# Performance work log

Measured on AMD Instinct MI355X. Metric: run time of the kernel, lower is better.

## Reference

```python
import jax, jax.numpy as jnp
import numpy as np

B, L, D = 8, 2048, 1024
MASKED = -2.0 ** 31  # fp32 path of the torch code


def setup_inputs() -> dict:
    key = jax.random.key(0)
    ks = jax.random.split(key, 11)
    s = 1.0 / np.sqrt(D)
    return {
        "Q": jax.random.normal(ks[0], (B, L, D), jnp.float32),
        "K": jax.random.normal(ks[1], (B, L, D), jnp.float32),
        "V": jax.random.normal(ks[2], (B, L, D), jnp.float32),
        "Wq": jax.random.normal(ks[3], (D, D), jnp.float32) * s,
        "bq": jax.random.normal(ks[4], (D,), jnp.float32) * s,
        "Wk": jax.random.normal(ks[5], (D, D), jnp.float32) * s,
        "bk": jax.random.normal(ks[6], (D,), jnp.float32) * s,
        "Wv": jax.random.normal(ks[7], (D, D), jnp.float32) * s,
        "bv": jax.random.normal(ks[8], (D,), jnp.float32) * s,
        "q_mask": jax.random.randint(ks[9], (B, L), 0, 2, jnp.int32),
        "k_mask": jax.random.randint(ks[10], (B, L), 0, 2, jnp.int32),
    }


def reference(Q, K, V, Wq, bq, Wk, bk, Wv, bv, q_mask, k_mask):
    # with_projection=True: linear projections (torch Linear: x @ W.T + b)
    Qp = jnp.einsum("bld,ed->ble", Q, Wq) + bq
    Kp = jnp.einsum("bld,ed->ble", K, Wk) + bk
    Vp = jnp.einsum("bld,ed->ble", V, Wv) + bv
    # NOTE: source hard-sets scale = 1 after computing sqrt(d_hidden)
    e = jnp.einsum("bqd,bkd->bqk", Qp, Kp)            # [B, Lq, Lk]
    e = jnp.where(k_mask[:, None, :] == 0, MASKED, e)  # masked_fill on key axis
    a = jax.nn.softmax(e, axis=-1)                     # with_sparse=False
    # dropout is identity in eval/reference mode
    a = jnp.einsum("bqk,bkd->bqd", a, Vp)
    a = jnp.where(q_mask[:, :, None] == 0, 0.0, a)     # zero masked query rows
    return a, e
```

## Files before the change

### kernel.cpp

```cpp
#include <hip/hip_runtime.h>
#include <cstddef>
#include <cstdint>

constexpr int Bn = 8;
constexpr int Ln = 2048;
constexpr int Dn = 1024;
constexpr float MASKED_VAL = -2147483648.0f;

typedef unsigned short u16;
typedef unsigned int   u32;
typedef __attribute__((ext_vector_type(8))) __bf16 bf16x8;
typedef __attribute__((ext_vector_type(4))) float  f32x4;

__device__ __forceinline__ u16 f2bf(float x) {
    u32 u = __float_as_uint(x);
    u += 0x7FFFu + ((u >> 16) & 1u);
    return (u16)(u >> 16);
}
__device__ __forceinline__ float bf2f(u16 h) {
    return __uint_as_float(((u32)h) << 16);
}
__device__ __forceinline__ u32 pack2(float a, float b) {
    return (u32)f2bf(a) | ((u32)f2bf(b) << 16);
}
__device__ __forceinline__ int rup(int x, int m) { return (x + m - 1) & ~(m - 1); }

__device__ __forceinline__ void gload16(const void* g, void* l) {
    typedef const __attribute__((address_space(1))) unsigned int* gp_t;
    typedef __attribute__((address_space(3))) unsigned int* lp_t;
    __builtin_amdgcn_global_load_lds((gp_t)g, (lp_t)l, 16, 0, 0);
}

#define MFMA16(a, b, c) __builtin_amdgcn_mfma_f32_16x16x32_bf16((a), (b), (c), 0, 0, 0)

__global__ __launch_bounds__(256) void prep_kernel(
    const int* __restrict__ k_mask, const int* __restrict__ q_mask,
    int* __restrict__ kidx, int* __restrict__ kpos,
    int* __restrict__ qidx, int* __restrict__ qpos, int* __restrict__ cnts)
{
    __shared__ int sc[256];
    __shared__ int lastv;
    const int b = blockIdx.x, t = threadIdx.x;
    for (int pass = 0; pass < 2; ++pass) {
        const int* msk = (pass ? q_mask : k_mask) + b * Ln;
        int* idx = (pass ? qidx : kidx) + b * Ln;
        int* pos = (pass ? qpos : kpos) + b * Ln;
        int f[8], s = 0;
        #pragma unroll
        for (int j = 0; j < 8; ++j) { f[j] = (msk[t * 8 + j] != 0) ? 1 : 0; s += f[j]; }
        sc[t] = s;
        __syncthreads();
        #pragma unroll
        for (int o = 1; o < 256; o <<= 1) {
            int v = (t >= o) ? sc[t - o] : 0;
            __syncthreads();
            sc[t] += v;
            __syncthreads();
        }
        int incl = sc[t];
        int total = sc[255];
        int p = incl - s;
        #pragma unroll
        for (int j = 0; j < 8; ++j) {
            pos[t * 8 + j] = f[j] ? p : -1;
            if (f[j]) { idx[p] = t * 8 + j; ++p; }
        }
        __syncthreads();
        if (t == 0) {
            cnts[b * 2 + pass] = total;
            lastv = (total > 0) ? idx[total - 1] : 0;
        }
        __syncthreads();
        int padv = (pass == 0) ? lastv : 0;
        for (int e2 = total + t; e2 < Ln; e2 += 256) idx[e2] = padv;
        __syncthreads();
    }
}

__global__ __launch_bounds__(256) void convert_single_kernel(
    const float* __restrict__ src, u16* __restrict__ dh, int n)
{
    int i = (blockIdx.x * 256 + threadIdx.x) * 8;
    if (i >= n) return;
    float f[8];
    *(float4*)&f[0] = *(const float4*)(src + i);
    *(float4*)&f[4] = *(const float4*)(src + i + 4);
    u32 H[4];
    #pragma unroll
    for (int j = 0; j < 4; ++j) H[j] = pack2(f[2*j], f[2*j+1]);
    *(uint4*)(dh + i) = make_uint4(H[0], H[1], H[2], H[3]);
}

__global__ __launch_bounds__(256) void convgather_kernel(
    const float* __restrict__ K, const float* __restrict__ V,
    const int* __restrict__ kidx, const int* __restrict__ cnts,
    u16* __restrict__ Xkc, u16* __restrict__ Vc)
{
    const int b = blockIdx.z, j = blockIdx.x, y = blockIdx.y;
    if (j >= rup(cnts[b * 2], 128)) return;
    const int src_row = kidx[b * Ln + j];
    const float* src = (y ? V : K) + ((size_t)b * Ln + src_row) * Dn;
    u16* dst = (y ? Vc : Xkc) + ((size_t)b * Ln + j) * Dn;
    const int t = threadIdx.x;
    float4 f = *(const float4*)(src + t * 4);
    *(uint2*)(dst + t * 4) = make_uint2(pack2(f.x, f.y), pack2(f.z, f.w));
}

__global__ __launch_bounds__(256) void wtrans_kernel(
    const float* __restrict__ Wq, const float* __restrict__ Wk,
    u16* __restrict__ Wqt, u16* __restrict__ Wkt)
{
    __shared__ float tile[64][68];
    const float* src = blockIdx.z ? Wk : Wq;
    u16* dst = blockIdx.z ? Wkt : Wqt;
    const int e0 = blockIdx.y * 64, d0 = blockIdx.x * 64;
    const int t = threadIdx.x;
    const int r = t >> 2, cq = (t & 3) * 16;
    const float* s = src + (size_t)(e0 + r) * Dn + d0 + cq;
    #pragma unroll
    for (int i = 0; i < 4; ++i)
        *(float4*)&tile[r][cq + i * 4] = *(const float4*)(s + i * 4);
    __syncthreads();
    u32 o[8];
    #pragma unroll
    for (int i = 0; i < 8; ++i)
        o[i] = pack2(tile[cq + 2 * i][r], tile[cq + 2 * i + 1][r]);
    u16* d = dst + (size_t)(d0 + r) * Dn + e0 + cq;
    *(uint4*)(d)     = make_uint4(o[0], o[1], o[2], o[3]);
    *(uint4*)(d + 8) = make_uint4(o[4], o[5], o[6], o[7]);
}

__global__ __launch_bounds__(64) void ck_kernel(
    const float* __restrict__ bq, const float* __restrict__ bk, float* __restrict__ cbuf)
{
    int l = threadIdx.x;
    float s = 0.f;
    #pragma unroll
    for (int i = 0; i < 16; ++i) s += bq[l + 64 * i] * bk[l + 64 * i];
    #pragma unroll
    for (int o = 32; o; o >>= 1) s += __shfl_xor(s, o, 64);
    if (l == 0) cbuf[0] = s;
}

__global__ __launch_bounds__(256) void wvec_kernel(
    const u16* __restrict__ Wqt, const u16* __restrict__ Wkt,
    const float* __restrict__ bk, const float* __restrict__ bq,
    float* __restrict__ w1, float* __restrict__ w2)
{
    const int y = blockIdx.y;
    const u16* src = y ? Wkt : Wqt;
    const float* vec = y ? bq : bk;
    float* out = y ? w2 : w1;
    const int d = blockIdx.x * 4 + (threadIdx.x >> 6);
    const int l = threadIdx.x & 63;
    float s = 0.f;
    #pragma unroll
    for (int i = 0; i < 16; ++i) {
        int e = l + 64 * i;
        s += bf2f(src[(size_t)d * Dn + e]) * vec[e];
    }
    #pragma unroll
    for (int o = 32; o; o >>= 1) s += __shfl_xor(s, o, 64);
    if (l == 0) out[d] = s;
}

__global__ __launch_bounds__(256) void rowdot_kernel(
    const u16* __restrict__ Xq, const u16* __restrict__ Xkc,
    const float* __restrict__ w1, const float* __restrict__ w2,
    const float* __restrict__ cbuf, float* __restrict__ u, float* __restrict__ vc)
{
    const int y = blockIdx.y;
    const u16* x = y ? Xkc : Xq;
    const float* w = y ? w2 : w1;
    float* out = y ? vc : u;
    const int row = blockIdx.x * 4 + (threadIdx.x >> 6);
    const int l = threadIdx.x & 63;
    float s = 0.f;
    #pragma unroll
    for (int h = 0; h < 2; ++h) {
        const u16* xp = x + (size_t)row * Dn + h * 512 + l * 8;
        const float* wp = w + h * 512 + l * 8;
        uint4 xv = *(const uint4*)xp;
        float4 wa = *(const float4*)(wp);
        float4 wb = *(const float4*)(wp + 4);
        const u16* xs = (const u16*)&xv;
        s += bf2f(xs[0]) * wa.x + bf2f(xs[1]) * wa.y + bf2f(xs[2]) * wa.z + bf2f(xs[3]) * wa.w
           + bf2f(xs[4]) * wb.x + bf2f(xs[5]) * wb.y + bf2f(xs[6]) * wb.z + bf2f(xs[7]) * wb.w;
    }
    #pragma unroll
    for (int o = 32; o; o >>= 1) s += __shfl_xor(s, o, 64);
    if (l == 0) out[row] = s + (y ? 0.0f : cbuf[0]);
}

__global__ __launch_bounds__(256) void zeroa_kernel(
    float4* __restrict__ out_a, const int* __restrict__ q_mask)
{
    const int row = blockIdx.x;
    if (q_mask[row]) return;
    out_a[(size_t)row * 256 + threadIdx.x] = make_float4(0.f, 0.f, 0.f, 0.f);
}

__global__ __launch_bounds__(256) void mgemm_kernel(
    const u16* __restrict__ Wkt, const u16* __restrict__ Wqt, u16* __restrict__ Mt)
{
    __shared__ __align__(16) unsigned char As[128 * 128];
    __shared__ __align__(16) unsigned char Bs[128 * 128];

    const int m0 = blockIdx.y * 128, n0 = blockIdx.x * 128;
    const int tid = threadIdx.x, lane = tid & 63, wid = tid >> 6;
    const int wm = (wid >> 1) * 64, wn = (wid & 1) * 64;

    const u16* gA[4]; const u16* gB[4]; int ldsOff[4];
    #pragma unroll
    for (int q = 0; q < 4; ++q) {
        int c = wid * 4 + q;
        int row = c * 8 + (lane >> 3);
        int sig = (lane & 7) ^ (row & 7);
        gA[q] = Wkt + (size_t)(m0 + row) * Dn + sig * 8;
        gB[q] = Wqt + (size_t)(n0 + row) * Dn + sig * 8;
        ldsOff[q] = c * 1024;
    }

    f32x4 acc[4][4];
    const f32x4 z4 = {0.f, 0.f, 0.f, 0.f};
    #pragma unroll
    for (int i = 0; i < 4; ++i)
        #pragma unroll
        for (int j = 0; j < 4; ++j) acc[i][j] = z4;

    for (int k0 = 0; k0 < Dn; k0 += 64) {
        #pragma unroll
        for (int q = 0; q < 4; ++q) {
            gload16(gA[q], As + ldsOff[q]);
            gload16(gB[q], Bs + ldsOff[q]);
            gA[q] += 64; gB[q] += 64;
        }
        __syncthreads();

        const int sh = lane >> 4;
        #pragma unroll
        for (int s = 0; s < 2; ++s) {
            bf16x8 af[4], bf[4];
            #pragma unroll
            for (int i = 0; i < 4; ++i) {
                int row = wm + i * 16 + (lane & 15);
                af[i] = *(const bf16x8*)(As + row * 128 + (((s * 4 + sh) ^ (row & 7)) << 4));
            }
            #pragma unroll
            for (int j = 0; j < 4; ++j) {
                int row = wn + j * 16 + (lane & 15);
                bf[j] = *(const bf16x8*)(Bs + row * 128 + (((s * 4 + sh) ^ (row & 7)) << 4));
            }
            #pragma unroll
            for (int i = 0; i < 4; ++i)
                #pragma unroll
                for (int j = 0; j < 4; ++j)
                    acc[i][j] = MFMA16(af[i], bf[j], acc[i][j]);
        }
        __syncthreads();
    }

    #pragma unroll
    for (int i = 0; i < 4; ++i) {
        #pragma unroll
        for (int r = 0; r < 4; ++r) {
            int m = m0 + wm + i * 16 + (lane >> 4) * 4 + r;
            u16* oh = Mt + (size_t)m * Dn + n0 + wn;
            #pragma unroll
            for (int j = 0; j < 4; ++j)
                oh[j * 16 + (lane & 15)] = f2bf(acc[i][j][r]);
        }
    }
}

__global__ __launch_bounds__(256) void proj2_kernel(
    const u16* __restrict__ Xq, const u16* __restrict__ Mt, u16* __restrict__ Tb)
{
    __shared__ __align__(16) unsigned char As[128 * 128];
    __shared__ __align__(16) unsigned char Bs[128 * 128];

    const int m0 = blockIdx.y * 128, n0 = blockIdx.x * 128;
    const int tid = threadIdx.x, lane = tid & 63, wid = tid >> 6;
    const int wm = (wid >> 1) * 64, wn = (wid & 1) * 64;

    const u16* gA[4]; const u16* gB[4]; int ldsOff[4];
    #pragma unroll
    for (int q = 0; q < 4; ++q) {
        int c = wid * 4 + q;
        int row = c * 8 + (lane >> 3);
        int sig = (lane & 7) ^ (row & 7);
        gA[q] = Xq + (size_t)(m0 + row) * Dn + sig * 8;
        gB[q] = Mt + (size_t)(n0 + row) * Dn + sig * 8;
        ldsOff[q] = c * 1024;
    }

    f32x4 acc[4][4];
    const f32x4 z4 = {0.f, 0.f, 0.f, 0.f};
    #pragma unroll
    for (int i = 0; i < 4; ++i)
        #pragma unroll
        for (int j = 0; j < 4; ++j) acc[i][j] = z4;

    for (int k0 = 0; k0 < Dn; k0 += 64) {
        #pragma unroll
        for (int q = 0; q < 4; ++q) {
            gload16(gA[q], As + ldsOff[q]);
            gload16(gB[q], Bs + ldsOff[q]);
            gA[q] += 64; gB[q] += 64;
        }
        __syncthreads();

        const int sh = lane >> 4;
        #pragma unroll
        for (int s = 0; s < 2; ++s) {
            bf16x8 af[4], bf[4];
            #pragma unroll
            for (int i = 0; i < 4; ++i) {
                int row = wm + i * 16 + (lane & 15);
                af[i] = *(const bf16x8*)(As + row * 128 + (((s * 4 + sh) ^ (row & 7)) << 4));
            }
            #pragma unroll
            for (int j = 0; j < 4; ++j) {
                int row = wn + j * 16 + (lane & 15);
                bf[j] = *(const bf16x8*)(Bs + row * 128 + (((s * 4 + sh) ^ (row & 7)) << 4));
            }
            #pragma unroll
            for (int i = 0; i < 4; ++i)
                #pragma unroll
                for (int j = 0; j < 4; ++j)
                    acc[i][j] = MFMA16(af[i], bf[j], acc[i][j]);
        }
        __syncthreads();
    }

    #pragma unroll
    for (int i = 0; i < 4; ++i) {
        #pragma unroll
        for (int r = 0; r < 4; ++r) {
            int m = m0 + wm + i * 16 + (lane >> 4) * 4 + r;
            u16* oh = Tb + (size_t)m * Dn + n0 + wn;
            #pragma unroll
            for (int j = 0; j < 4; ++j)
                oh[j * 16 + (lane & 15)] = f2bf(acc[i][j][r]);
        }
    }
}

__global__ __launch_bounds__(256) void projv_kernel(
    const u16* __restrict__ Vc, const u16* __restrict__ Wvb,
    const float* __restrict__ bv, const int* __restrict__ cnts,
    u16* __restrict__ Vhc)
{
    __shared__ __align__(16) unsigned char As[128 * 128];
    __shared__ __align__(16) unsigned char Bs[128 * 128];

    const int b = blockIdx.z;
    const int kc_b = cnts[b * 2];
    const int m0 = blockIdx.y * 128;
    if (m0 >= rup(kc_b, 128)) return;
    const int n0 = blockIdx.x * 128;
    const int tid = threadIdx.x, lane = tid & 63, wid = tid >> 6;
    const int wm = (wid >> 1) * 64, wn = (wid & 1) * 64;

    const u16* Vc_b = Vc + (size_t)b * Ln * Dn;

    const u16* gA[4]; const u16* gB[4]; int ldsOff[4];
    #pragma unroll
    for (int q = 0; q < 4; ++q) {
        int c = wid * 4 + q;
        int row = c * 8 + (lane >> 3);
        int sig = (lane & 7) ^ (row & 7);
        gA[q] = Vc_b + (size_t)(m0 + row) * Dn + sig * 8;
        gB[q] = Wvb + (size_t)(n0 + row) * Dn + sig * 8;
        ldsOff[q] = c * 1024;
    }

    f32x4 acc[4][4];
    const f32x4 z4 = {0.f, 0.f, 0.f, 0.f};
    #pragma unroll
    for (int i = 0; i < 4; ++i)
        #pragma unroll
        for (int j = 0; j < 4; ++j) acc[i][j] = z4;

    for (int k0 = 0; k0 < Dn; k0 += 64) {
        #pragma unroll
        for (int q = 0; q < 4; ++q) {
            gload16(gA[q], As + ldsOff[q]);
            gload16(gB[q], Bs + ldsOff[q]);
            gA[q] += 64; gB[q] += 64;
        }
        __syncthreads();

        const int sh = lane >> 4;
        #pragma unroll
        for (int s = 0; s < 2; ++s) {
            bf16x8 af[4], bf[4];
            #pragma unroll
            for (int i = 0; i < 4; ++i) {
                int row = wm + i * 16 + (lane & 15);
                af[i] = *(const bf16x8*)(As + row * 128 + (((s * 4 + sh) ^ (row & 7)) << 4));
            }
            #pragma unroll
            for (int j = 0; j < 4; ++j) {
                int row = wn + j * 16 + (lane & 15);
                bf[j] = *(const bf16x8*)(Bs + row * 128 + (((s * 4 + sh) ^ (row & 7)) << 4));
            }
            #pragma unroll
            for (int i = 0; i < 4; ++i)
                #pragma unroll
                for (int j = 0; j < 4; ++j)
                    acc[i][j] = MFMA16(af[i], bf[j], acc[i][j]);
        }
        __syncthreads();
    }

    float bv4[4];
    #pragma unroll
    for (int j = 0; j < 4; ++j) bv4[j] = bv[n0 + wn + j * 16 + (lane & 15)];
    u16* Vhc_b = Vhc + (size_t)b * Ln * Dn;
    #pragma unroll
    for (int i = 0; i < 4; ++i) {
        #pragma unroll
        for (int r = 0; r < 4; ++r) {
            int m = m0 + wm + i * 16 + (lane >> 4) * 4 + r;
            u16* oh = Vhc_b + (size_t)m * Dn + n0 + wn;
            #pragma unroll
            for (int j = 0; j < 4; ++j)
                oh[j * 16 + (lane & 15)] = f2bf(acc[i][j][r] + bv4[j]);
        }
    }
}

__global__ __launch_bounds__(256) void vtransc_kernel(
    const u16* __restrict__ Vhc, const int* __restrict__ cnts,
    u16* __restrict__ Vtc)
{
    __shared__ u16 tile[64][72];
    const int b = blockIdx.z;
    const int l0 = blockIdx.y * 64, d0 = blockIdx.x * 64;
    if (l0 >= rup(cnts[b * 2], 64)) return;
    const int t = threadIdx.x;
    const int r = t >> 2, cq = (t & 3) * 16;

    const u16* src = Vhc + (size_t)(b * Ln + l0 + r) * Dn + d0 + cq;
    *(uint4*)&tile[r][cq]     = *(const uint4*)(src);
    *(uint4*)&tile[r][cq + 8] = *(const uint4*)(src + 8);
    __syncthreads();

    u16 tmp[16];
    #pragma unroll
    for (int i = 0; i < 16; ++i) tmp[i] = tile[cq + i][r];
    u16* dst = Vtc + (size_t)b * Dn * Ln + (size_t)(d0 + r) * Ln + l0 + cq;
    *(uint4*)(dst)     = *(uint4*)&tmp[0];
    *(uint4*)(dst + 8) = *(uint4*)&tmp[8];
}

__global__ __launch_bounds__(256) void scorec_kernel(
    const u16* __restrict__ Tb, const u16* __restrict__ Xkc,
    const int* __restrict__ cnts,
    const float* __restrict__ u, const float* __restrict__ vc,
    u16* __restrict__ Ec)
{
    __shared__ __align__(16) unsigned char As[128 * 128];
    __shared__ __align__(16) unsigned char Bs[128 * 128];

    const int d = blockIdx.x;
    const int f = (d & 7) * 256 + (d >> 3);
    const int b = f >> 8;
    const int rem = f & 255;
    const int m0 = (rem >> 4) * 128;
    const int n0 = (rem & 15) * 128;

    const int kc_b = cnts[b * 2];
    if (n0 >= kc_b) return;
    const int tid = threadIdx.x, lane = tid & 63, wid = tid >> 6;
    const int wm = (wid >> 1) * 64, wn = (wid & 1) * 64;

    const size_t boff = (size_t)b * Ln * Dn;
    const u16* Tb_b  = Tb  + boff;
    const u16* Xkc_b = Xkc + boff;

    const u16* gA[4]; const u16* gB[4]; int ldsOff[4];
    #pragma unroll
    for (int q = 0; q < 4; ++q) {
        int c = wid * 4 + q;
        int row = c * 8 + (lane >> 3);
        int sig = (lane & 7) ^ (row & 7);
        gA[q] = Tb_b  + (size_t)(m0 + row) * Dn + sig * 8;
        gB[q] = Xkc_b + (size_t)(n0 + row) * Dn + sig * 8;
        ldsOff[q] = c * 1024;
    }

    f32x4 acc[4][4];
    const f32x4 z4 = {0.f, 0.f, 0.f, 0.f};
    #pragma unroll
    for (int i = 0; i < 4; ++i)
        #pragma unroll
        for (int j = 0; j < 4; ++j) acc[i][j] = z4;

    for (int k0 = 0; k0 < Dn; k0 += 64) {
        #pragma unroll
        for (int q = 0; q < 4; ++q) {
            gload16(gA[q], As + ldsOff[q]);
            gload16(gB[q], Bs + ldsOff[q]);
            gA[q] += 64; gB[q] += 64;
        }
        __syncthreads();

        const int sh = lane >> 4;
        #pragma unroll
        for (int s = 0; s < 2; ++s) {
            bf16x8 af[4], bf[4];
            #pragma unroll
            for (int i = 0; i < 4; ++i) {
                int row = wm + i * 16 + (lane & 15);
                af[i] = *(const bf16x8*)(As + row * 128 + (((s * 4 + sh) ^ (row & 7)) << 4));
            }
            #pragma unroll
            for (int j = 0; j < 4; ++j) {
                int row = wn + j * 16 + (lane & 15);
                bf[j] = *(const bf16x8*)(Bs + row * 128 + (((s * 4 + sh) ^ (row & 7)) << 4));
            }
            #pragma unroll
            for (int i = 0; i < 4; ++i)
                #pragma unroll
                for (int j = 0; j < 4; ++j)
                    acc[i][j] = MFMA16(af[i], bf[j], acc[i][j]);
        }
        __syncthreads();
    }

    float vcl[4];
    #pragma unroll
    for (int j = 0; j < 4; ++j) vcl[j] = vc[b * Ln + n0 + wn + j * 16 + (lane & 15)];
    #pragma unroll
    for (int i = 0; i < 4; ++i) {
        #pragma unroll
        for (int r = 0; r < 4; ++r) {
            int m = m0 + wm + i * 16 + (lane >> 4) * 4 + r;
            float um = u[b * Ln + m];
            u16* orow = Ec + ((size_t)(b * Ln + m)) * Ln + n0 + wn;
            #pragma unroll
            for (int j = 0; j < 4; ++j) {
                int jj = n0 + wn + j * 16 + (lane & 15);
                orow[j * 16 + (lane & 15)] =
                    f2bf((jj < kc_b) ? (acc[i][j][r] + um + vcl[j]) : MASKED_VAL);
            }
        }
    }
}

__global__ __launch_bounds__(256) void stats_expand_kernel(
    const u16* __restrict__ Ec, const int* __restrict__ kpos,
    const int* __restrict__ qpos, const int* __restrict__ cnts,
    u16* __restrict__ Pc, float* __restrict__ e)
{
    __shared__ float redm[4];
    __shared__ float reds[4];
    const int row = blockIdx.x;
    const int b = row >> 11;
    const int t = threadIdx.x;
    const u16* er = Ec + (size_t)row * Ln;
    const int qp = qpos[row];

    if (qp >= 0) {
        const int bound = rup(cnts[b * 2], 64);
        const int lane = t & 63, wave = t >> 6;
        float v[8];
        int base = t * 8;
        if (base < bound) {
            uint4 x = *(const uint4*)(er + base);
            const u16* xs = (const u16*)&x;
            #pragma unroll
            for (int j = 0; j < 8; ++j) v[j] = bf2f(xs[j]);
        } else {
            #pragma unroll
            for (int j = 0; j < 8; ++j) v[j] = MASKED_VAL;
        }

        float mx = v[0];
        #pragma unroll
        for (int j = 1; j < 8; ++j) mx = fmaxf(mx, v[j]);
        #pragma unroll
        for (int o = 32; o > 0; o >>= 1) mx = fmaxf(mx, __shfl_xor(mx, o, 64));
        if (lane == 0) redm[wave] = mx;
        __syncthreads();
        mx = fmaxf(fmaxf(redm[0], redm[1]), fmaxf(redm[2], redm[3]));

        float s = 0.f;
        #pragma unroll
        for (int j = 0; j < 8; ++j) s += __expf(v[j] - mx);
        #pragma unroll
        for (int o = 32; o > 0; o >>= 1) s += __shfl_xor(s, o, 64);
        if (lane == 0) reds[wave] = s;
        __syncthreads();
        s = reds[0] + reds[1] + reds[2] + reds[3];
        float sinv = 1.0f / s;

        u32 P[4];
        #pragma unroll
        for (int j = 0; j < 4; ++j)
            P[j] = pack2(__expf(v[2*j] - mx) * sinv, __expf(v[2*j+1] - mx) * sinv);
        u16* pr = Pc + ((size_t)b * Ln + qp) * Ln + t * 8;
        *(uint4*)pr = make_uint4(P[0], P[1], P[2], P[3]);
    }

    const int* kp = kpos + b * Ln;
    const int k = t * 8;
    int p[8];
    *(int4*)&p[0] = *(const int4*)(kp + k);
    *(int4*)&p[4] = *(const int4*)(kp + k + 4);
    float o[8];
    #pragma unroll
    for (int j = 0; j < 8; ++j)
        o[j] = (p[j] >= 0) ? bf2f(er[p[j]]) : MASKED_VAL;

    float* eo = e + (size_t)row * Ln + k;
    *(float4*)(eo)     = make_float4(o[0], o[1], o[2], o[3]);
    *(float4*)(eo + 4) = make_float4(o[4], o[5], o[6], o[7]);
}

__global__ __launch_bounds__(256) void pvc_kernel(
    const u16* __restrict__ Pc, const u16* __restrict__ Vtc,
    const int* __restrict__ qidx, const int* __restrict__ cnts,
    float* __restrict__ out_a)
{
    __shared__ __align__(16) unsigned char As[128 * 128];
    __shared__ __align__(16) unsigned char Bs[128 * 128];

    const int d = blockIdx.x;
    const int f = (d & 7) * 128 + (d >> 3);
    const int b = f >> 7;
    const int rem = f & 127;
    const int m0 = (rem >> 3) * 128;
    const int n0 = (rem & 7) * 128;

    const int kc_b = cnts[b * 2], qc_b = cnts[b * 2 + 1];
    if (m0 >= rup(qc_b, 128)) return;
    const int kbound = rup(kc_b, 64);
    const int tid = threadIdx.x, lane = tid & 63, wid = tid >> 6;
    const int wm = (wid >> 1) * 64, wn = (wid & 1) * 64;

    const u16* Pc_b  = Pc  + (size_t)b * Ln * Ln;
    const u16* Vtc_b = Vtc + (size_t)b * Dn * Ln;
    const int* qidx_b = qidx + b * Ln;

    const u16* gA[4]; const u16* gB[4]; int ldsOff[4];
    #pragma unroll
    for (int q = 0; q < 4; ++q) {
        int c = wid * 4 + q;
        int row = c * 8 + (lane >> 3);
        int sig = (lane & 7) ^ (row & 7);
        gA[q] = Pc_b  + (size_t)(m0 + row) * Ln + sig * 8;
        gB[q] = Vtc_b + (size_t)(n0 + row) * Ln + sig * 8;
        ldsOff[q] = c * 1024;
    }

    f32x4 acc[4][4];
    const f32x4 z4 = {0.f, 0.f, 0.f, 0.f};
    #pragma unroll
    for (int i = 0; i < 4; ++i)
        #pragma unroll
        for (int j = 0; j < 4; ++j) acc[i][j] = z4;

    for (int k0 = 0; k0 < kbound; k0 += 64) {
        #pragma unroll
        for (int q = 0; q < 4; ++q) {
            gload16(gA[q], As + ldsOff[q]);
            gload16(gB[q], Bs + ldsOff[q]);
            gA[q] += 64; gB[q] += 64;
        }
        __syncthreads();

        const int sh = lane >> 4;
        #pragma unroll
        for (int s = 0; s < 2; ++s) {
            bf16x8 af[4], bv[4];
            #pragma unroll
            for (int i = 0; i < 4; ++i) {
                int row = wm + i * 16 + (lane & 15);
                af[i] = *(const bf16x8*)(As + row * 128 + (((s * 4 + sh) ^ (row & 7)) << 4));
            }
            #pragma unroll
            for (int j = 0; j < 4; ++j) {
                int row = wn + j * 16 + (lane & 15);
                bv[j] = *(const bf16x8*)(Bs + row * 128 + (((s * 4 + sh) ^ (row & 7)) << 4));
            }
            #pragma unroll
            for (int i = 0; i < 4; ++i)
                #pragma unroll
                for (int j = 0; j < 4; ++j)
                    acc[i][j] = MFMA16(af[i], bv[j], acc[i][j]);
        }
        __syncthreads();
    }

    #pragma unroll
    for (int i = 0; i < 4; ++i) {
        #pragma unroll
        for (int r = 0; r < 4; ++r) {
            int gi = m0 + wm + i * 16 + (lane >> 4) * 4 + r;
            if (gi < qc_b) {
                int gm = qidx_b[gi];
                float* orow = out_a + (size_t)(b * Ln + gm) * Dn + n0 + wn;
                #pragma unroll
                for (int j = 0; j < 4; ++j)
                    orow[j * 16 + (lane & 15)] = acc[i][j][r];
            }
        }
    }
}

extern "C" void kernel_launch(void* const* d_in, const int* in_sizes, int n_in,
                              void* d_out, int out_size, void* d_ws, size_t ws_size,
                              hipStream_t stream)
{
    const float* Q  = (const float*)d_in[0];
    const float* K  = (const float*)d_in[1];
    const float* V  = (const float*)d_in[2];
    const float* Wq = (const float*)d_in[3];
    const float* bq = (const float*)d_in[4];
    const float* Wk = (const float*)d_in[5];
    const float* bk = (const float*)d_in[6];
    const float* Wv = (const float*)d_in[7];
    const float* bv = (const float*)d_in[8];
    const int* q_mask = (const int*)d_in[9];
    const int* k_mask = (const int*)d_in[10];

    float* out_a = (float*)d_out;
    float* out_e = out_a + (size_t)Bn * Ln * Dn;

    const size_t NE = (size_t)Bn * Ln * Dn;
    const size_t NW = (size_t)Dn * Dn;
    const int BL = Bn * Ln;

    u16* Vc  = (u16*)d_ws;
    u16* Xq  = Vc + NE;
    u16* Tb  = Xq + NE;
    u16* Vhc = Tb + NE;
    u16* Xkc = Vhc + NE;
    u16* Vtc = Xkc + NE;
    u16* Wvb = Vtc + NE;
    u16* Wqt = Wvb + NW;
    u16* Wkt = Wqt + NW;
    u16* Mt  = Wkt + NW;
    float* w1    = (float*)(Mt + NW);
    float* w2    = w1 + Dn;
    float* cbuf  = w2 + Dn;
    float* uarr  = cbuf + 4;
    float* vc    = uarr + BL;
    int* kidx = (int*)(vc + BL);
    int* kpos = kidx + BL;
    int* qidx = kpos + BL;
    int* qpos = qidx + BL;
    int* cnts = qpos + BL;

    u16* Ec = Vc;
    u16* Pc = Tb;

    dim3 blk(256);

    prep_kernel<<<dim3(Bn), blk, 0, stream>>>(k_mask, q_mask, kidx, kpos, qidx, qpos, cnts);

    convert_single_kernel<<<dim3(NE / 2048), blk, 0, stream>>>(Q, Xq, (int)NE);
    convgather_kernel<<<dim3(Ln, 2, Bn), blk, 0, stream>>>(K, V, kidx, cnts, Xkc, Vc);
    convert_single_kernel<<<dim3(NW / 2048), blk, 0, stream>>>(Wv, Wvb, (int)NW);

    wtrans_kernel<<<dim3(16, 16, 2), blk, 0, stream>>>(Wq, Wk, Wqt, Wkt);
    ck_kernel<<<dim3(1), dim3(64), 0, stream>>>(bq, bk, cbuf);
    wvec_kernel<<<dim3(256, 2), blk, 0, stream>>>(Wqt, Wkt, bk, bq, w1, w2);

    mgemm_kernel<<<dim3(8, 8), blk, 0, stream>>>(Wkt, Wqt, Mt);

    proj2_kernel<<<dim3(Dn / 128, BL / 128), blk, 0, stream>>>(Xq, Mt, Tb);
    projv_kernel<<<dim3(Dn / 128, Ln / 128, Bn), blk, 0, stream>>>(
        Vc, Wvb, bv, cnts, Vhc);

    rowdot_kernel<<<dim3(BL / 4, 2), blk, 0, stream>>>(Xq, Xkc, w1, w2, cbuf, uarr, vc);

    vtransc_kernel<<<dim3(Dn / 64, Ln / 64, Bn), blk, 0, stream>>>(Vhc, cnts, Vtc);

    scorec_kernel<<<dim3(2048), blk, 0, stream>>>(Tb, Xkc, cnts, uarr, vc, Ec);

    stats_expand_kernel<<<dim3(BL), blk, 0, stream>>>(Ec, kpos, qpos, cnts, Pc, out_e);

    zeroa_kernel<<<dim3(BL), blk, 0, stream>>>((float4*)out_a, q_mask);
    pvc_kernel<<<dim3(1024), blk, 0, stream>>>(Pc, Vtc, qidx, cnts, out_a);
}
```

Measured before the change: 356.7 us.

## Project compacted keys through combined weight instead of all queries

The combined weight product is now applied to the compacted (unmasked) key rows rather than to every query row, so the second projection GEMM skips tiles beyond each batch's unmasked-key count. The score GEMM then multiplies the raw queries by this projected-key buffer. About half the keys are masked, so roughly half the projection GEMM work is meant to go away. The workspace layout and buffer aliasing are reordered to match.

```diff
diff --git a/kernel.cpp b/kernel.cpp
--- a/kernel.cpp
+++ b/kernel.cpp
@@ -201,7 +201,7 @@
 }
 
 __global__ __launch_bounds__(256) void mgemm_kernel(
-    const u16* __restrict__ Wkt, const u16* __restrict__ Wqt, u16* __restrict__ Mt)
+    const u16* __restrict__ A, const u16* __restrict__ B, u16* __restrict__ C)
 {
     __shared__ __align__(16) unsigned char As[128 * 128];
     __shared__ __align__(16) unsigned char Bs[128 * 128];
@@ -216,8 +216,8 @@
         int c = wid * 4 + q;
         int row = c * 8 + (lane >> 3);
         int sig = (lane & 7) ^ (row & 7);
-        gA[q] = Wkt + (size_t)(m0 + row) * Dn + sig * 8;
-        gB[q] = Wqt + (size_t)(n0 + row) * Dn + sig * 8;
+        gA[q] = A + (size_t)(m0 + row) * Dn + sig * 8;
+        gB[q] = B + (size_t)(n0 + row) * Dn + sig * 8;
         ldsOff[q] = c * 1024;
     }
 
@@ -265,7 +265,7 @@
         #pragma unroll
         for (int r = 0; r < 4; ++r) {
             int m = m0 + wm + i * 16 + (lane >> 4) * 4 + r;
-            u16* oh = Mt + (size_t)m * Dn + n0 + wn;
+            u16* oh = C + (size_t)m * Dn + n0 + wn;
             #pragma unroll
             for (int j = 0; j < 4; ++j)
                 oh[j * 16 + (lane & 15)] = f2bf(acc[i][j][r]);
@@ -273,83 +273,9 @@
     }
 }
 
-__global__ __launch_bounds__(256) void proj2_kernel(
-    const u16* __restrict__ Xq, const u16* __restrict__ Mt, u16* __restrict__ Tb)
-{
-    __shared__ __align__(16) unsigned char As[128 * 128];
-    __shared__ __align__(16) unsigned char Bs[128 * 128];
-
-    const int m0 = blockIdx.y * 128, n0 = blockIdx.x * 128;
-    const int tid = threadIdx.x, lane = tid & 63, wid = tid >> 6;
-    const int wm = (wid >> 1) * 64, wn = (wid & 1) * 64;
-
-    const u16* gA[4]; const u16* gB[4]; int ldsOff[4];
-    #pragma unroll
-    for (int q = 0; q < 4; ++q) {
-        int c = wid * 4 + q;
-        int row = c * 8 + (lane >> 3);
-        int sig = (lane & 7) ^ (row & 7);
-        gA[q] = Xq + (size_t)(m0 + row) * Dn + sig * 8;
-        gB[q] = Mt + (size_t)(n0 + row) * Dn + sig * 8;
-        ldsOff[q] = c * 1024;
-    }
-
-    f32x4 acc[4][4];
-    const f32x4 z4 = {0.f, 0.f, 0.f, 0.f};
-    #pragma unroll
-    for (int i = 0; i < 4; ++i)
-        #pragma unroll
-        for (int j = 0; j < 4; ++j) acc[i][j] = z4;
-
-    for (int k0 = 0; k0 < Dn; k0 += 64) {
-        #pragma unroll
-        for (int q = 0; q < 4; ++q) {
-            gload16(gA[q], As + ldsOff[q]);
-            gload16(gB[q], Bs + ldsOff[q]);
-            gA[q] += 64; gB[q] += 64;
-        }
-        __syncthreads();
-
-        const int sh = lane >> 4;
-        #pragma unroll
-        for (int s = 0; s < 2; ++s) {
-            bf16x8 af[4], bf[4];
-            #pragma unroll
-            for (int i = 0; i < 4; ++i) {
-                int row = wm + i * 16 + (lane & 15);
-                af[i] = *(const bf16x8*)(As + row * 128 + (((s * 4 + sh) ^ (row & 7)) << 4));
-            }
-            #pragma unroll
-            for (int j = 0; j < 4; ++j) {
-                int row = wn + j * 16 + (lane & 15);
-                bf[j] = *(const bf16x8*)(Bs + row * 128 + (((s * 4 + sh) ^ (row & 7)) << 4));
-            }
-            #pragma unroll
-            for (int i = 0; i < 4; ++i)
-                #pragma unroll
-                for (int j = 0; j < 4; ++j)
-                    acc[i][j] = MFMA16(af[i], bf[j], acc[i][j]);
-        }
-        __syncthreads();
-    }
-
-    #pragma unroll
-    for (int i = 0; i < 4; ++i) {
-        #pragma unroll
-        for (int r = 0; r < 4; ++r) {
-            int m = m0 + wm + i * 16 + (lane >> 4) * 4 + r;
-            u16* oh = Tb + (size_t)m * Dn + n0 + wn;
-            #pragma unroll
-            for (int j = 0; j < 4; ++j)
-                oh[j * 16 + (lane & 15)] = f2bf(acc[i][j][r]);
-        }
-    }
-}
-
-__global__ __launch_bounds__(256) void projv_kernel(
-    const u16* __restrict__ Vc, const u16* __restrict__ Wvb,
-    const float* __restrict__ bv, const int* __restrict__ cnts,
-    u16* __restrict__ Vhc)
+__global__ __launch_bounds__(256) void gt_kernel(
+    const u16* __restrict__ Xkc, const u16* __restrict__ Mb,
+    const int* __restrict__ cnts, u16* __restrict__ Gt)
 {
     __shared__ __align__(16) unsigned char As[128 * 128];
     __shared__ __align__(16) unsigned char Bs[128 * 128];
@@ -362,6 +288,88 @@
     const int tid = threadIdx.x, lane = tid & 63, wid = tid >> 6;
     const int wm = (wid >> 1) * 64, wn = (wid & 1) * 64;
 
+    const u16* Xkc_b = Xkc + (size_t)b * Ln * Dn;
+
+    const u16* gA[4]; const u16* gB[4]; int ldsOff[4];
+    #pragma unroll
+    for (int q = 0; q < 4; ++q) {
+        int c = wid * 4 + q;
+        int row = c * 8 + (lane >> 3);
+        int sig = (lane & 7) ^ (row & 7);
+        gA[q] = Xkc_b + (size_t)(m0 + row) * Dn + sig * 8;
+        gB[q] = Mb + (size_t)(n0 + row) * Dn + sig * 8;
+        ldsOff[q] = c * 1024;
+    }
+
+    f32x4 acc[4][4];
+    const f32x4 z4 = {0.f, 0.f, 0.f, 0.f};
+    #pragma unroll
+    for (int i = 0; i < 4; ++i)
+        #pragma unroll
+        for (int j = 0; j < 4; ++j) acc[i][j] = z4;
+
+    for (int k0 = 0; k0 < Dn; k0 += 64) {
+        #pragma unroll
+        for (int q = 0; q < 4; ++q) {
+            gload16(gA[q], As + ldsOff[q]);
+            gload16(gB[q], Bs + ldsOff[q]);
+            gA[q] += 64; gB[q] += 64;
+        }
+        __syncthreads();
+
+        const int sh = lane >> 4;
+        #pragma unroll
+        for (int s = 0; s < 2; ++s) {
+            bf16x8 af[4], bf[4];
+            #pragma unroll
+            for (int i = 0; i < 4; ++i) {
+                int row = wm + i * 16 + (lane & 15);
+                af[i] = *(const bf16x8*)(As + row * 128 + (((s * 4 + sh) ^ (row & 7)) << 4));
+            }
+            #pragma unroll
+            for (int j = 0; j < 4; ++j) {
+                int row = wn + j * 16 + (lane & 15);
+                bf[j] = *(const bf16x8*)(Bs + row * 128 + (((s * 4 + sh) ^ (row & 7)) << 4));
+            }
+            #pragma unroll
+            for (int i = 0; i < 4; ++i)
+                #pragma unroll
+                for (int j = 0; j < 4; ++j)
+                    acc[i][j] = MFMA16(af[i], bf[j], acc[i][j]);
+        }
+        __syncthreads();
+    }
+
+    u16* Gt_b = Gt + (size_t)b * Ln * Dn;
+    #pragma unroll
+    for (int i = 0; i < 4; ++i) {
+        #pragma unroll
+        for (int r = 0; r < 4; ++r) {
+            int m = m0 + wm + i * 16 + (lane >> 4) * 4 + r;
+            u16* oh = Gt_b + (size_t)m * Dn + n0 + wn;
+            #pragma unroll
+            for (int j = 0; j < 4; ++j)
+                oh[j * 16 + (lane & 15)] = f2bf(acc[i][j][r]);
+        }
+    }
+}
+
+__global__ __launch_bounds__(256) void projv_kernel(
+    const u16* __restrict__ Vc, const u16* __restrict__ Wvb,
+    const float* __restrict__ bv, const int* __restrict__ cnts,
+    u16* __restrict__ Vhc)
+{
+    __shared__ __align__(16) unsigned char As[128 * 128];
+    __shared__ __align__(16) unsigned char Bs[128 * 128];
+
+    const int b = blockIdx.z;
+    const int kc_b = cnts[b * 2];
+    const int m0 = blockIdx.y * 128;
+    if (m0 >= rup(kc_b, 128)) return;
+    const int n0 = blockIdx.x * 128;
+    const int tid = threadIdx.x, lane = tid & 63, wid = tid >> 6;
+    const int wm = (wid >> 1) * 64, wn = (wid & 1) * 64;
+
     const u16* Vc_b = Vc + (size_t)b * Ln * Dn;
 
     const u16* gA[4]; const u16* gB[4]; int ldsOff[4];
@@ -456,7 +464,7 @@
 }
 
 __global__ __launch_bounds__(256) void scorec_kernel(
-    const u16* __restrict__ Tb, const u16* __restrict__ Xkc,
+    const u16* __restrict__ Xq, const u16* __restrict__ Gt,
     const int* __restrict__ cnts,
     const float* __restrict__ u, const float* __restrict__ vc,
     u16* __restrict__ Ec)
@@ -477,8 +485,8 @@
     const int wm = (wid >> 1) * 64, wn = (wid & 1) * 64;
 
     const size_t boff = (size_t)b * Ln * Dn;
-    const u16* Tb_b  = Tb  + boff;
-    const u16* Xkc_b = Xkc + boff;
+    const u16* Xq_b = Xq + boff;
+    const u16* Gt_b = Gt + boff;
 
     const u16* gA[4]; const u16* gB[4]; int ldsOff[4];
     #pragma unroll
@@ -486,8 +494,8 @@
         int c = wid * 4 + q;
         int row = c * 8 + (lane >> 3);
         int sig = (lane & 7) ^ (row & 7);
-        gA[q] = Tb_b  + (size_t)(m0 + row) * Dn + sig * 8;
-        gB[q] = Xkc_b + (size_t)(n0 + row) * Dn + sig * 8;
+        gA[q] = Xq_b + (size_t)(m0 + row) * Dn + sig * 8;
+        gB[q] = Gt_b + (size_t)(n0 + row) * Dn + sig * 8;
         ldsOff[q] = c * 1024;
     }
 
@@ -735,16 +743,16 @@
     const int BL = Bn * Ln;
 
     u16* Vc  = (u16*)d_ws;
-    u16* Xq  = Vc + NE;
-    u16* Tb  = Xq + NE;
-    u16* Vhc = Tb + NE;
-    u16* Xkc = Vhc + NE;
-    u16* Vtc = Xkc + NE;
+    u16* Xkc = Vc + NE;
+    u16* Gt  = Xkc + NE;
+    u16* Vhc = Gt + NE;
+    u16* Xq  = Vhc + NE;
+    u16* Vtc = Xq + NE;
     u16* Wvb = Vtc + NE;
     u16* Wqt = Wvb + NW;
     u16* Wkt = Wqt + NW;
-    u16* Mt  = Wkt + NW;
-    float* w1    = (float*)(Mt + NW);
+    u16* Mb  = Wkt + NW;
+    float* w1    = (float*)(Mb + NW);
     float* w2    = w1 + Dn;
     float* cbuf  = w2 + Dn;
     float* uarr  = cbuf + 4;
@@ -756,7 +764,7 @@
     int* cnts = qpos + BL;
 
     u16* Ec = Vc;
-    u16* Pc = Tb;
+    u16* Pc = Gt;
 
     dim3 blk(256);
 
@@ -770,9 +778,9 @@
     ck_kernel<<<dim3(1), dim3(64), 0, stream>>>(bq, bk, cbuf);
     wvec_kernel<<<dim3(256, 2), blk, 0, stream>>>(Wqt, Wkt, bk, bq, w1, w2);
 
-    mgemm_kernel<<<dim3(8, 8), blk, 0, stream>>>(Wkt, Wqt, Mt);
-
-    proj2_kernel<<<dim3(Dn / 128, BL / 128), blk, 0, stream>>>(Xq, Mt, Tb);
+    mgemm_kernel<<<dim3(8, 8), blk, 0, stream>>>(Wqt, Wkt, Mb);
+
+    gt_kernel<<<dim3(Dn / 128, Ln / 128, Bn), blk, 0, stream>>>(Xkc, Mb, cnts, Gt);
     projv_kernel<<<dim3(Dn / 128, Ln / 128, Bn), blk, 0, stream>>>(
         Vc, Wvb, bv, cnts, Vhc);
 
@@ -780,7 +788,7 @@
 
     vtransc_kernel<<<dim3(Dn / 64, Ln / 64, Bn), blk, 0, stream>>>(Vhc, cnts, Vtc);
 
-    scorec_kernel<<<dim3(2048), blk, 0, stream>>>(Tb, Xkc, cnts, uarr, vc, Ec);
+    scorec_kernel<<<dim3(2048), blk, 0, stream>>>(Xq, Gt, cnts, uarr, vc, Ec);
 
     stats_expand_kernel<<<dim3(BL), blk, 0, stream>>>(Ec, kpos, qpos, cnts, Pc, out_e);
 
```

Result: faster. 339.8 us (-4.8%).
